# Kernel tuning notes

Hardware: AMD Instinct MI355X
Metric: run time of the kernel (lower is better)

The kernel has to match this reference:

```python
import jax, jax.numpy as jnp
import numpy as np

# ---- model constants (match init_kwargs) ----
N_USERS = 100_000
N_ITEMS = 50_000
N_ENTITIES = 200_000          # items are entities [0, N_ITEMS)
N_REL = 20                    # relations after the +1 shift; rel_weight has N_REL-1 rows
EMB = 64
HOPS = 2
MARGIN_CCL = 0.8
NUM_NEG = 64
ANGLE_W = 0.1
ANGLE_DROP = 0.5              # eval-mode Dropout(ones)*rate == constant rate scaling
N_EDGES = 1_000_000
NNZ = 1_000_000
N_TRIPLETS = 200_000
BATCH = 4096
EPS = 1e-6


def _l2norm(x):
    # torch F.normalize(dim=-1, eps=1e-12)
    return x / jnp.maximum(jnp.linalg.norm(x, axis=-1, keepdims=True), 1e-12)


def setup_inputs() -> dict:
    key = jax.random.key(0)
    ks = jax.random.split(key, 13)
    # xavier_uniform bounds: sqrt(6/(fan_in+fan_out))
    b_all = float(np.sqrt(6.0 / (N_USERS + N_ENTITIES + EMB)))
    b_cf = float(np.sqrt(6.0 / (N_ITEMS + EMB)))
    b_rel = float(np.sqrt(6.0 / (N_REL - 1 + EMB)))
    all_embed = jax.random.uniform(ks[0], (N_USERS + N_ENTITIES, EMB), jnp.float32, -b_all, b_all)
    item_emb_cf = jax.random.uniform(ks[1], (N_ITEMS, EMB), jnp.float32, -b_cf, b_cf)
    rel_weight = jax.random.uniform(ks[2], (N_REL - 1, EMB), jnp.float32, -b_rel, b_rel)
    # D^{-1/2} A row-normalized positive values
    interact_vals = jax.random.uniform(ks[3], (NNZ,), jnp.float32, 0.01, 0.3)
    user = jax.random.randint(ks[4], (BATCH,), 0, N_USERS)
    pos_item = jax.random.randint(ks[5], (BATCH,), 0, N_ITEMS)
    neg_item = jax.random.randint(ks[6], (BATCH, NUM_NEG), 0, N_ITEMS)
    edge_index = jax.random.randint(ks[7], (2, N_EDGES), 0, N_ENTITIES)
    edge_type = jax.random.randint(ks[8], (N_EDGES,), 1, N_REL)  # relations already +1 shifted
    interact_rows = jax.random.randint(ks[9], (NNZ,), 0, N_USERS)
    interact_cols = jax.random.randint(ks[10], (NNZ,), 0, N_ITEMS)  # URM cols live in item range
    triplet_h = jax.random.randint(ks[11], (N_TRIPLETS,), 0, N_ENTITIES)
    triplet_t = jax.random.randint(ks[12], (N_TRIPLETS,), 0, N_ITEMS)
    return dict(all_embed=all_embed, item_emb_cf=item_emb_cf, rel_weight=rel_weight,
                interact_vals=interact_vals, user=user, pos_item=pos_item, neg_item=neg_item,
                edge_index=edge_index, edge_type=edge_type, interact_rows=interact_rows,
                interact_cols=interact_cols, triplet_h=triplet_h, triplet_t=triplet_t)


def _gcn(user_emb, entity_emb, item_cf, rel_weight, edge_index, edge_type, rows, cols, vals):
    """Multi-hop HAKG GraphConv: relation-gated KG scatter-mean + sparse user/CF aggregation."""
    head, tail = edge_index[0], edge_index[1]
    ent_res, usr_res, cf_res = entity_emb, user_emb, item_cf
    cnt = jax.ops.segment_sum(jnp.ones(head.shape, entity_emb.dtype), head, N_ENTITIES)
    denom = jnp.maximum(cnt, 1.0)[:, None]            # scatter_mean denominator
    rel_e = rel_weight[edge_type - 1]                 # [E, D]
    for _ in range(HOPS):
        # KG aggregate: entity_agg[h] = mean_{(h,r,t)} entity[t] * rel[r]
        neigh = entity_emb[tail] * rel_e              # [E, D]
        entity_agg = jax.ops.segment_sum(neigh, head, N_ENTITIES) / denom
        # user aggregate: sparse interact_mat @ entity_emb
        user_agg = jax.ops.segment_sum(vals[:, None] * entity_emb[cols], rows, N_USERS)
        # CF branch (LightGCN-style): R @ item_cf then R^T @ (...)
        u_cf = jax.ops.segment_sum(vals[:, None] * item_cf[cols], rows, N_USERS)
        item_agg_cf = jax.ops.segment_sum(vals[:, None] * u_cf[rows], cols, N_ITEMS)
        entity_emb = _l2norm(entity_agg)
        user_emb = _l2norm(user_agg)
        item_cf = _l2norm(item_agg_cf)
        ent_res = ent_res + entity_emb
        usr_res = usr_res + user_emb
        cf_res = cf_res + item_cf
    return ent_res, usr_res, cf_res


def _half_aperture(u):
    K = 0.1
    sqnu = jnp.clip(jnp.sum(u * u, -1), 0.0, 1.0 - EPS)
    return jnp.arcsin(jnp.clip(K * (1.0 - sqnu) / jnp.sqrt(sqnu), -1.0 + EPS, 1.0 - EPS))


def _angle_at_u(u, v):
    nu = jnp.linalg.norm(u, axis=-1)
    nv = jnp.linalg.norm(v, axis=-1)
    dp = jnp.sum(u * v, -1)
    ed = jnp.linalg.norm(u - v, axis=-1)
    num = dp * (1.0 + nu ** 2) - nu ** 2 * (1.0 + nv ** 2)
    den = nu * ed * jnp.sqrt(jnp.clip(1.0 + nv ** 2 * nu ** 2 - 2.0 * dp, EPS, None)) + EPS
    return jnp.arccos(jnp.clip(num / den, -1.0 + EPS, 1.0 - EPS))


def _contrastive_loss(u_e, pos_e, neg_e, pos_cf, neg_cf):
    B = u_e.shape[0]
    u, p, n = _l2norm(u_e), _l2norm(pos_e), _l2norm(neg_e)
    pcf, ncf = _l2norm(pos_cf), _l2norm(neg_cf)
    ui_pos = jax.nn.relu(2.0 - (jnp.sum(u * p, -1) + jnp.sum(u * pcf, -1)))
    ub = jnp.repeat(u, NUM_NEG, axis=0)               # [B*K, D]
    def neg_loss(nn_):
        s = jax.nn.relu(jnp.sum(ub * nn_, -1) - MARGIN_CCL).reshape(B, NUM_NEG)
        return jnp.sum(s, -1) / (jnp.sum(s > 0, -1).astype(s.dtype) + 1e-5)
    return jnp.mean(ui_pos + neg_loss(n) + neg_loss(ncf))


def reference(all_embed, item_emb_cf, rel_weight, interact_vals, user, pos_item, neg_item,
              edge_index, edge_type, interact_rows, interact_cols, triplet_h, triplet_t):
    user_emb = all_embed[:N_USERS]
    entity_emb = all_embed[N_USERS:]
    ent_g, usr_g, cf_g = _gcn(user_emb, entity_emb, item_emb_cf, rel_weight,
                              edge_index, edge_type, interact_rows, interact_cols, interact_vals)
    flat_neg = neg_item.reshape(-1)
    u_e = usr_g[user]
    loss1 = _contrastive_loss(u_e, ent_g[pos_item], ent_g[flat_neg], cf_g[pos_item], cf_g[flat_neg])
    # angle (hierarchy) loss, vectorized over all cross-type triplets
    hs = entity_emb[triplet_h] * ANGLE_DROP
    ts = entity_emb[triplet_t] * ANGLE_DROP
    angle_half = jax.nn.relu(_angle_at_u(hs, ts) - _half_aperture(hs))
    loss2 = ANGLE_W * jnp.sum(angle_half) / N_TRIPLETS
    return loss1 + loss2
```

## Files before the change

### kernel.cpp

```cpp
#include <hip/hip_runtime.h>
#include <math.h>

#define N_USERS    100000
#define N_ITEMS    50000
#define N_ENTITIES 200000
#define N_REL      20
#define EMB        64
#define HOPS       2
#define MARGIN_CCL 0.8f
#define NUM_NEG    64
#define ANGLE_W    0.1f
#define ANGLE_DROP 0.5f
#define N_EDGES    1000000
#define NNZ        1000000
#define N_TRIPLETS 200000
#define BATCH      4096
#define EPSF       1e-6f

#define TILE1 4096
#define NBUCK 196
#define ACAP  8192
#define HBLK  ((N_EDGES + TILE1 - 1) / TILE1)
#define P1B   (3 * HBLK)
#define KGB   (N_ENTITIES / 32)
#define UCFB  (N_USERS / 32)
#define ITEMB ((N_ITEMS + 31) / 32)
#define UBB   (BATCH / 32)
#define ANGB  (N_TRIPLETS / 32)
#define LOSSB (BATCH / 4)
#define CONVE (N_ENTITIES * 16 / 256)
#define CONVI (N_ITEMS * 16 / 256)

typedef _Float16 half4_t __attribute__((ext_vector_type(4)));
typedef _Float16 half8_t __attribute__((ext_vector_type(8)));
typedef float float8_t __attribute__((ext_vector_type(8)));

__device__ inline float4 h2f(half4_t h) {
    return make_float4((float)h.x, (float)h.y, (float)h.z, (float)h.w);
}
__device__ inline half4_t f2h(float4 f) {
    half4_t h; h.x = (_Float16)f.x; h.y = (_Float16)f.y;
    h.z = (_Float16)f.z; h.w = (_Float16)f.w; return h;
}
__device__ inline float8_t h8_to_f8(half8_t h) { return __builtin_convertvector(h, float8_t); }
__device__ inline half8_t f8_to_h8(float8_t f) { return __builtin_convertvector(f, half8_t); }
__device__ inline half8_t h8_zero() {
    half8_t z;
    #pragma unroll
    for (int i = 0; i < 8; ++i) z[i] = (_Float16)0.0f;
    return z;
}
__device__ inline float sum_sq8(float8_t f) {
    float s = 0.f;
    #pragma unroll
    for (int i = 0; i < 8; ++i) s += f[i] * f[i];
    return s;
}
__device__ inline float dot8(float8_t a, float8_t b) {
    float s = 0.f;
    #pragma unroll
    for (int i = 0; i < 8; ++i) s += a[i] * b[i];
    return s;
}
__device__ inline float8_t f8_from2(float4 lo, float4 hi) {
    float8_t f;
    f[0] = lo.x; f[1] = lo.y; f[2] = lo.z; f[3] = lo.w;
    f[4] = hi.x; f[5] = hi.y; f[6] = hi.z; f[7] = hi.w;
    return f;
}
__device__ inline float grp_red8(float v) {
    v += __shfl_xor(v, 1, 64); v += __shfl_xor(v, 2, 64); v += __shfl_xor(v, 4, 64);
    return v;
}
__device__ inline float dot4(float4 a, float4 b) {
    return a.x * b.x + a.y * b.y + a.z * b.z + a.w * b.w;
}
__device__ inline float grp_red16(float v) {
    v += __shfl_xor(v, 1, 64); v += __shfl_xor(v, 2, 64);
    v += __shfl_xor(v, 4, 64); v += __shfl_xor(v, 8, 64);
    return v;
}
__device__ inline float cross_grp_scalar(float v) {
    v += __shfl_xor(v, 16, 64); v += __shfl_xor(v, 32, 64);
    return v;
}
__device__ inline int f32_to_h16bits(float v) {
    _Float16 h = (_Float16)v;
    return (int)__builtin_bit_cast(unsigned short, h);
}
__device__ inline _Float16 h16_from_bits(int b) {
    return __builtin_bit_cast(_Float16, (unsigned short)(b & 0xFFFF));
}

__global__ void __launch_bounds__(256) prep_kernel(
        int* __restrict__ bcur_e, int* __restrict__ bcur_u, int* __restrict__ bcur_i) {
    int t = threadIdx.x;
    if (t < NBUCK) {
        bcur_e[t] = t * ACAP;
        bcur_u[t] = t * ACAP;
        bcur_i[t] = t * ACAP;
    }
}

__device__ inline void angle_body(int ablk, int t, const half8_t* __restrict__ ent_h,
                                  const int* __restrict__ th, const int* __restrict__ tt,
                                  float* sb, float* __restrict__ l2blk) {
    int o = t & 7;
    int grp = t >> 3;
    int trip = ablk * 32 + grp;
    int h = th[trip], t2 = tt[trip];
    float8_t hv = h8_to_f8(ent_h[h * 8 + o]);
    float8_t tv = h8_to_f8(ent_h[t2 * 8 + o]);
    hv *= ANGLE_DROP;
    tv *= ANGLE_DROP;
    float8_t dv = hv - tv;
    float s_hh = grp_red8(sum_sq8(hv));
    float s_tt = grp_red8(sum_sq8(tv));
    float s_ht = grp_red8(dot8(hv, tv));
    float s_dd = grp_red8(sum_sq8(dv));
    if (o == 0) {
        float nu = sqrtf(s_hh);
        float ed = sqrtf(s_dd);
        float sqnu = fminf(fmaxf(s_hh, 0.0f), 1.0f - EPSF);
        float ha_arg = fminf(fmaxf(0.1f * (1.0f - sqnu) / sqrtf(sqnu), -1.0f + EPSF), 1.0f - EPSF);
        float half_ap = asinf(ha_arg);
        float num = s_ht * (1.0f + s_hh) - s_hh * (1.0f + s_tt);
        float den = nu * ed * sqrtf(fmaxf(1.0f + s_tt * s_hh - 2.0f * s_ht, EPSF)) + EPSF;
        float ang = acosf(fminf(fmaxf(num / den, -1.0f + EPSF), 1.0f - EPSF));
        sb[grp] = fmaxf(ang - half_ap, 0.0f);
    }
    __syncthreads();
    if (t == 0) {
        float tot = 0.f;
        #pragma unroll
        for (int i = 0; i < 32; ++i) tot += sb[i];
        l2blk[ablk] = tot;
    }
}

__global__ void __launch_bounds__(256) phase1_sort(
        const int* __restrict__ head, const int* __restrict__ tail,
        const int* __restrict__ etype, const int* __restrict__ rows,
        const int* __restrict__ cols, const float* __restrict__ vals,
        int* __restrict__ bcur_e, int* __restrict__ bcur_u, int* __restrict__ bcur_i,
        int* __restrict__ keys_ping, int* __restrict__ kg_ping,
        int2* __restrict__ u_ping, int2* __restrict__ i_ping,
        const float4* __restrict__ ent0, const float4* __restrict__ cf0,
        half4_t* __restrict__ ent_a4, half4_t* __restrict__ cf16a4) {
    __shared__ int2 pay_st[TILE1];
    __shared__ int lhist[256], lstart[256], lcur[256], gbase[256];
    __shared__ int wsum[4], wpre[4];
    int bx = blockIdx.x, t = threadIdx.x;
    if (bx >= P1B) {
        int cb = bx - P1B;
        if (cb < CONVE) { int i = cb * 256 + t; ent_a4[i] = f2h(ent0[i]); }
        else            { int i = (cb - CONVE) * 256 + t; cf16a4[i] = f2h(cf0[i]); }
        return;
    }
    int seg = bx / HBLK;
    int tb  = bx % HBLK;
    int tstart = tb * TILE1;
    int valid = min(TILE1, N_EDGES - tstart);
    const int* karr = (seg == 0) ? head : (seg == 1) ? rows : cols;
    int shift = (seg == 0) ? 10 : (seg == 1) ? 9 : 8;
    int* bcur = (seg == 0) ? bcur_e : (seg == 1) ? bcur_u : bcur_i;
    lhist[t] = 0;
    __syncthreads();
    for (int i = t; i < valid; i += 256) atomicAdd(&lhist[karr[tstart + i] >> shift], 1);
    __syncthreads();
    int v = lhist[t];
    int lane = t & 63, wv = t >> 6;
    int sc = v;
    #pragma unroll
    for (int d = 1; d < 64; d <<= 1) {
        int x = __shfl_up(sc, d, 64);
        if (lane >= d) sc += x;
    }
    if (lane == 63) wsum[wv] = sc;
    __syncthreads();
    if (t == 0) {
        int a = 0;
        #pragma unroll
        for (int i = 0; i < 4; ++i) { wpre[i] = a; a += wsum[i]; }
    }
    __syncthreads();
    int excl = sc + wpre[wv] - v;
    lstart[t] = excl;
    lcur[t] = excl;
    gbase[t] = atomicAdd(&bcur[t], v);
    __syncthreads();
    if (seg == 0) {
        int* key_st = (int*)pay_st;
        int* ps = key_st + TILE1;
        for (int i = t; i < valid; i += 256) {
            int h = head[tstart + i];
            int p = tail[tstart + i] | ((etype[tstart + i] - 1) << 18);
            int sp = atomicAdd(&lcur[h >> 10], 1);
            key_st[sp] = h;
            ps[sp] = p;
        }
        __syncthreads();
        for (int j = t; j < valid; j += 256) {
            int k = key_st[j];
            int b = k >> 10;
            int pos = gbase[b] + (j - lstart[b]);
            keys_ping[pos] = k;
            kg_ping[pos] = ps[j];
        }
    } else {
        int2* pay = (seg == 1) ? u_ping : i_ping;
        for (int i = t; i < valid; i += 256) {
            int k = karr[tstart + i];
            int bkt = k >> shift;
            int px;
            if (seg == 1) px = cols[tstart + i] | ((k & 511) << 16);
            else          px = rows[tstart + i] | ((k & 255) << 17);
            int py = f32_to_h16bits(vals[tstart + i]) | (bkt << 16);
            int sp = atomicAdd(&lcur[bkt], 1);
            pay_st[sp] = make_int2(px, py);
        }
        __syncthreads();
        for (int j = t; j < valid; j += 256) {
            int2 p = pay_st[j];
            int bb = (p.y >> 16) & 0xFF;
            int pos = gbase[bb] + (j - lstart[bb]);
            pay[pos] = p;
        }
    }
}

__global__ void __launch_bounds__(256) phase2_all(
        const int* __restrict__ bcur_e, const int* __restrict__ keys_ping,
        const int* __restrict__ kg_ping, int* __restrict__ kg_pack, int* __restrict__ off_e,
        const int* __restrict__ bcur_u, const int2* __restrict__ u_ping,
        int2* __restrict__ u_pack, int* __restrict__ off_u,
        const int* __restrict__ bcur_i, const int2* __restrict__ i_ping,
        int2* __restrict__ i_pack, int* __restrict__ off_i) {
    __shared__ int hist[1024];
    __shared__ int wsum[4], wpre[4];
    int seg = blockIdx.x / NBUCK;
    int b   = blockIdx.x % NBUCK;
    int t = threadIdx.x;
    int bins  = (seg == 0) ? 1024 : (seg == 1) ? 512 : 256;
    int shift = (seg == 0) ? 10 : (seg == 1) ? 9 : 8;
    int n_rows = (seg == 0) ? N_ENTITIES : (seg == 1) ? N_USERS : N_ITEMS;
    const int* bcur = (seg == 0) ? bcur_e : (seg == 1) ? bcur_u : bcur_i;
    int* off = (seg == 0) ? off_e : (seg == 1) ? off_u : off_i;
    int rs = b << shift;
    int re = min(rs + bins, n_rows);
    int nr = re - rs;
    int base = b * ACAP;
    int len = bcur[b] - base;
    for (int r = t; r < bins; r += 256) hist[r] = 0;
    __syncthreads();
    if (seg == 0) {
        for (int j = t; j < len; j += 256) atomicAdd(&hist[keys_ping[base + j] - rs], 1);
    } else if (seg == 1) {
        for (int j = t; j < len; j += 256) atomicAdd(&hist[(u_ping[base + j].x >> 16) & 511], 1);
    } else {
        for (int j = t; j < len; j += 256) atomicAdd(&hist[(i_ping[base + j].x >> 17) & 255], 1);
    }
    __syncthreads();
    int own = bins >> 8;
    int c[4]; int tot = 0;
    #pragma unroll
    for (int i = 0; i < 4; ++i) { c[i] = (i < own) ? hist[t * own + i] : 0; tot += c[i]; }
    int lane = t & 63, wv = t >> 6;
    int sc = tot;
    #pragma unroll
    for (int d = 1; d < 64; d <<= 1) {
        int x = __shfl_up(sc, d, 64);
        if (lane >= d) sc += x;
    }
    if (lane == 63) wsum[wv] = sc;
    __syncthreads();
    if (t == 0) {
        int a = 0;
        #pragma unroll
        for (int i = 0; i < 4; ++i) { wpre[i] = a; a += wsum[i]; }
    }
    __syncthreads();
    int run = sc + wpre[wv] - tot;
    #pragma unroll
    for (int i = 0; i < 4; ++i) { if (i < own) { hist[t * own + i] = run; run += c[i]; } }
    __syncthreads();
    for (int r = t; r < nr; r += 256) off[rs + b + r] = base + hist[r];
    if (t == 0) off[rs + b + nr] = base + len;
    __syncthreads();
    if (seg == 0) {
        for (int j = t; j < len; j += 256) {
            int k = keys_ping[base + j];
            int slot = atomicAdd(&hist[k - rs], 1);
            kg_pack[base + slot] = kg_ping[base + j];
        }
    } else if (seg == 1) {
        for (int j = t; j < len; j += 256) {
            int2 p = u_ping[base + j];
            int slot = atomicAdd(&hist[(p.x >> 16) & 511], 1);
            u_pack[base + slot] = p;
        }
    } else {
        for (int j = t; j < len; j += 256) {
            int2 p = i_ping[base + j];
            int slot = atomicAdd(&hist[(p.x >> 17) & 255], 1);
            i_pack[base + slot] = p;
        }
    }
}

__device__ inline void kg0_body(int bid, int t, const int* __restrict__ off,
                                const int* __restrict__ pack, half8_t* srel,
                                const float* __restrict__ relw,
                                const half8_t* __restrict__ src, half8_t* __restrict__ dst,
                                half8_t* __restrict__ res, const float4* __restrict__ res_init) {
    if (t < (N_REL - 1) * 8) {
        int rel = t >> 3, o = t & 7;
        const float4* r4 = (const float4*)relw;
        srel[rel * 9 + o] = f8_to_h8(f8_from2(r4[rel * 16 + o * 2], r4[rel * 16 + o * 2 + 1]));
    }
    __syncthreads();
    int row = bid * 32 + (t >> 3);
    int o = t & 7;
    int idx = row + (row >> 10);
    int s = off[idx], e = off[idx + 1];
    half8_t acc = h8_zero();
    int k = s;
    for (; k + 2 <= e; k += 2) {
        int p0 = pack[k], p1 = pack[k + 1];
        half8_t a0 = src[(p0 & 0x3FFFF) * 8 + o];
        half8_t b0 = srel[(p0 >> 18) * 9 + o];
        half8_t a1 = src[(p1 & 0x3FFFF) * 8 + o];
        half8_t b1 = srel[(p1 >> 18) * 9 + o];
        acc += a0 * b0;
        acc += a1 * b1;
    }
    if (k < e) {
        int p0 = pack[k];
        acc += src[(p0 & 0x3FFFF) * 8 + o] * srel[(p0 >> 18) * 9 + o];
    }
    float8_t f = h8_to_f8(acc);
    f *= 1.0f / fmaxf((float)(e - s), 1.0f);
    float ss = grp_red8(sum_sq8(f));
    f *= 1.0f / fmaxf(sqrtf(ss), 1e-12f);
    dst[row * 8 + o] = f8_to_h8(f);
    if (row < N_ITEMS) {
        float8_t rr = f8_from2(res_init[row * 16 + o * 2], res_init[row * 16 + o * 2 + 1]);
        rr += f;
        res[row * 8 + o] = f8_to_h8(rr);
    }
}

__device__ inline void kg2_body(int bid, int t, const int* __restrict__ off,
                                const int* __restrict__ pack, half8_t* srel,
                                const float* __restrict__ relw,
                                const half8_t* __restrict__ src, half8_t* __restrict__ res) {
    if (t < (N_REL - 1) * 8) {
        int rel = t >> 3, o = t & 7;
        const float4* r4 = (const float4*)relw;
        srel[rel * 9 + o] = f8_to_h8(f8_from2(r4[rel * 16 + o * 2], r4[rel * 16 + o * 2 + 1]));
    }
    __syncthreads();
    int row = bid * 32 + (t >> 3);
    if (row >= N_ITEMS) return;
    int o = t & 7;
    int idx = row + (row >> 10);
    int s = off[idx], e = off[idx + 1];
    half8_t acc = h8_zero();
    int k = s;
    for (; k + 2 <= e; k += 2) {
        int p0 = pack[k], p1 = pack[k + 1];
        half8_t a0 = src[(p0 & 0x3FFFF) * 8 + o];
        half8_t b0 = srel[(p0 >> 18) * 9 + o];
        half8_t a1 = src[(p1 & 0x3FFFF) * 8 + o];
        half8_t b1 = srel[(p1 >> 18) * 9 + o];
        acc += a0 * b0;
        acc += a1 * b1;
    }
    if (k < e) {
        int p0 = pack[k];
        acc += src[(p0 & 0x3FFFF) * 8 + o] * srel[(p0 >> 18) * 9 + o];
    }
    float8_t f = h8_to_f8(acc);
    f *= 1.0f / fmaxf((float)(e - s), 1.0f);
    float ss = grp_red8(sum_sq8(f));
    f *= 1.0f / fmaxf(sqrtf(ss), 1e-12f);
    float8_t rr = h8_to_f8(res[row * 8 + o]);
    rr += f;
    float s2 = grp_red8(sum_sq8(rr));
    rr *= 1.0f / fmaxf(sqrtf(s2), 1e-12f);
    res[row * 8 + o] = f8_to_h8(rr);
}

__device__ inline void ucf_body(int bid, int t, const int* __restrict__ off,
                                const int2* __restrict__ u_pack,
                                const half8_t* __restrict__ cf16,
                                half8_t* __restrict__ ucf) {
    int row = bid * 32 + (t >> 3);
    int o = t & 7;
    int idx = row + (row >> 9);
    int s = off[idx], e = off[idx + 1];
    half8_t acc = h8_zero();
    int k = s;
    for (; k + 2 <= e; k += 2) {
        int2 p0 = u_pack[k], p1 = u_pack[k + 1];
        _Float16 v0 = h16_from_bits(p0.y);
        _Float16 v1 = h16_from_bits(p1.y);
        acc += cf16[(p0.x & 0xFFFF) * 8 + o] * v0;
        acc += cf16[(p1.x & 0xFFFF) * 8 + o] * v1;
    }
    if (k < e) {
        int2 p0 = u_pack[k];
        acc += cf16[(p0.x & 0xFFFF) * 8 + o] * h16_from_bits(p0.y);
    }
    ucf[row * 8 + o] = acc;
}

__device__ inline void ubatch_body(int bid, int t, const int* __restrict__ user,
                                   const int* __restrict__ off,
                                   const int2* __restrict__ u_pack,
                                   const half8_t* __restrict__ ent_a,
                                   const half8_t* __restrict__ ent_b,
                                   const float4* __restrict__ usr0f,
                                   half8_t* __restrict__ usr_b) {
    int g = t >> 3, o = t & 7;
    int b = bid * 32 + g;
    int uid = user[b];
    int idx = uid + (uid >> 9);
    int s = off[idx], e = off[idx + 1];
    half8_t acc1 = h8_zero(), acc2 = h8_zero();
    int k = s;
    for (; k + 2 <= e; k += 2) {
        int2 p0 = u_pack[k], p1 = u_pack[k + 1];
        int c0 = (p0.x & 0xFFFF) * 8 + o;
        int c1 = (p1.x & 0xFFFF) * 8 + o;
        _Float16 v0 = h16_from_bits(p0.y);
        _Float16 v1 = h16_from_bits(p1.y);
        acc1 += ent_a[c0] * v0;
        acc2 += ent_b[c0] * v0;
        acc1 += ent_a[c1] * v1;
        acc2 += ent_b[c1] * v1;
    }
    if (k < e) {
        int2 p0 = u_pack[k];
        int c0 = (p0.x & 0xFFFF) * 8 + o;
        _Float16 v0 = h16_from_bits(p0.y);
        acc1 += ent_a[c0] * v0;
        acc2 += ent_b[c0] * v0;
    }
    float8_t f1 = h8_to_f8(acc1);
    float ss1 = grp_red8(sum_sq8(f1));
    f1 *= 1.0f / fmaxf(sqrtf(ss1), 1e-12f);
    float8_t u0 = f8_from2(usr0f[uid * 16 + o * 2], usr0f[uid * 16 + o * 2 + 1]);
    float8_t r1 = h8_to_f8(f8_to_h8(u0 + f1));
    float8_t f2 = h8_to_f8(acc2);
    float ss2 = grp_red8(sum_sq8(f2));
    f2 *= 1.0f / fmaxf(sqrtf(ss2), 1e-12f);
    float8_t r = r1 + f2;
    float s3 = grp_red8(sum_sq8(r));
    r *= 1.0f / fmaxf(sqrtf(s3), 1e-12f);
    usr_b[b * 8 + o] = f8_to_h8(r);
}

__device__ inline void item_body(int bid, int t, const int* __restrict__ off,
                                 const int2* __restrict__ i_pack,
                                 const half8_t* __restrict__ ucf,
                                 half8_t* __restrict__ cf_nxt, half8_t* __restrict__ res,
                                 const float4* __restrict__ res_init, int first, int last) {
    int row = bid * 32 + (t >> 3);
    int o = t & 7;
    if (row >= N_ITEMS) return;
    int idx = row + (row >> 8);
    int s = off[idx], e = off[idx + 1];
    half8_t acc = h8_zero();
    int k = s;
    for (; k + 2 <= e; k += 2) {
        int2 p0 = i_pack[k], p1 = i_pack[k + 1];
        _Float16 v0 = h16_from_bits(p0.y);
        _Float16 v1 = h16_from_bits(p1.y);
        acc += ucf[(p0.x & 0x1FFFF) * 8 + o] * v0;
        acc += ucf[(p1.x & 0x1FFFF) * 8 + o] * v1;
    }
    if (k < e) {
        int2 p0 = i_pack[k];
        acc += ucf[(p0.x & 0x1FFFF) * 8 + o] * h16_from_bits(p0.y);
    }
    float8_t f = h8_to_f8(acc);
    float ss = grp_red8(sum_sq8(f));
    f *= 1.0f / fmaxf(sqrtf(ss), 1e-12f);
    if (!last) cf_nxt[row * 8 + o] = f8_to_h8(f);
    float8_t rr;
    if (first) rr = f8_from2(res_init[row * 16 + o * 2], res_init[row * 16 + o * 2 + 1]);
    else       rr = h8_to_f8(res[row * 8 + o]);
    rr += f;
    if (last) {
        float s2 = grp_red8(sum_sq8(rr));
        rr *= 1.0f / fmaxf(sqrtf(s2), 1e-12f);
    }
    res[row * 8 + o] = f8_to_h8(rr);
}

__device__ inline void loss_ent_body(int b, int t,
                                     const int* __restrict__ pos, const int* __restrict__ neg,
                                     const half4_t* __restrict__ usrb4,
                                     const half4_t* __restrict__ ent4,
                                     float* __restrict__ dpe, float* __restrict__ l1pe) {
    int lane = t & 63;
    int g = lane >> 4, q = lane & 15;
    int pid = pos[b];
    float4 u = h2f(usrb4[b * 16 + q]);
    float4 p = h2f(ent4[pid * 16 + q]);
    float dpe_v = grp_red16(dot4(u, p));
    float sum_n = 0.f, cnt_n = 0.f;
    const int* nb = neg + b * NUM_NEG;
    for (int j = 0; j < NUM_NEG; j += 8) {
        int n0 = nb[j + g], n1 = nb[j + 4 + g];
        float dn0 = grp_red16(dot4(u, h2f(ent4[n0 * 16 + q])));
        float dn1 = grp_red16(dot4(u, h2f(ent4[n1 * 16 + q])));
        float s0 = fmaxf(dn0 - MARGIN_CCL, 0.f); sum_n += s0; if (s0 > 0.f) cnt_n += 1.f;
        float s1 = fmaxf(dn1 - MARGIN_CCL, 0.f); sum_n += s1; if (s1 > 0.f) cnt_n += 1.f;
    }
    sum_n = cross_grp_scalar(sum_n); cnt_n = cross_grp_scalar(cnt_n);
    if (lane == 0) {
        dpe[b] = dpe_v;
        l1pe[b] = sum_n / (cnt_n + 1e-5f);
    }
}

__global__ void __launch_bounds__(256) loss_cf_kernel(
        const int* __restrict__ pos, const int* __restrict__ neg,
        const half4_t* __restrict__ usrb4, const half4_t* __restrict__ cf4,
        const float* __restrict__ dpe, const float* __restrict__ l1pe,
        float* __restrict__ l1p) {
    int b = blockIdx.x * 4 + (threadIdx.x >> 6);
    int lane = threadIdx.x & 63;
    int g = lane >> 4, q = lane & 15;
    int pid = pos[b];
    float4 u = h2f(usrb4[b * 16 + q]);
    float4 pc = h2f(cf4[pid * 16 + q]);
    float dpc = grp_red16(dot4(u, pc));
    float sum_c = 0.f, cnt_c = 0.f;
    const int* nb = neg + b * NUM_NEG;
    for (int j = 0; j < NUM_NEG; j += 8) {
        int n0 = nb[j + g], n1 = nb[j + 4 + g];
        float dc0 = grp_red16(dot4(u, h2f(cf4[n0 * 16 + q])));
        float dc1 = grp_red16(dot4(u, h2f(cf4[n1 * 16 + q])));
        float t0 = fmaxf(dc0 - MARGIN_CCL, 0.f); sum_c += t0; if (t0 > 0.f) cnt_c += 1.f;
        float t1 = fmaxf(dc1 - MARGIN_CCL, 0.f); sum_c += t1; if (t1 > 0.f) cnt_c += 1.f;
    }
    sum_c = cross_grp_scalar(sum_c); cnt_c = cross_grp_scalar(cnt_c);
    if (lane == 0) {
        float ui_pos = fmaxf(2.0f - dpe[b] - dpc, 0.0f);
        l1p[b] = ui_pos + l1pe[b] + sum_c / (cnt_c + 1e-5f);
    }
}

__global__ void __launch_bounds__(256) fused_h0(
        const int* __restrict__ off_e, const int* __restrict__ kg_pack,
        const float* __restrict__ relw, const half8_t* __restrict__ ent_a,
        half8_t* __restrict__ ent_b, half8_t* __restrict__ ent_res,
        const float4* __restrict__ ent0f,
        const int* __restrict__ off_u, const int2* __restrict__ u_pack,
        const half8_t* __restrict__ cf16_a, half8_t* __restrict__ ucf,
        const int* __restrict__ th, const int* __restrict__ tt,
        float* __restrict__ l2blk) {
    __shared__ half8_t srel[(N_REL - 1) * 9];
    __shared__ float sb[32];
    int bx = blockIdx.x, t = threadIdx.x;
    if (bx < KGB) {
        kg0_body(bx, t, off_e, kg_pack, srel, relw, ent_a, ent_b, ent_res, ent0f);
    } else if (bx < KGB + UCFB) {
        ucf_body(bx - KGB, t, off_u, u_pack, cf16_a, ucf);
    } else {
        angle_body(bx - KGB - UCFB, t, ent_a, th, tt, sb, l2blk);
    }
}

__global__ void __launch_bounds__(256) fused_ik(
        const int* __restrict__ off_e, const int* __restrict__ kg_pack,
        const float* __restrict__ relw, const half8_t* __restrict__ ent_b,
        half8_t* __restrict__ ent_res,
        const int* __restrict__ off_i, const int2* __restrict__ i_pack,
        const half8_t* __restrict__ ucf, half8_t* __restrict__ cf16_b,
        half8_t* __restrict__ cf_res, const float4* __restrict__ cf0f,
        const int* __restrict__ user, const int* __restrict__ off_u,
        const int2* __restrict__ u_pack, const half8_t* __restrict__ ent_a,
        const float4* __restrict__ usr0f, half8_t* __restrict__ usr_b) {
    __shared__ half8_t srel[(N_REL - 1) * 9];
    int bx = blockIdx.x, t = threadIdx.x;
    if (bx < ITEMB) {
        kg2_body(bx, t, off_e, kg_pack, srel, relw, ent_b, ent_res);
    } else if (bx < 2 * ITEMB) {
        item_body(bx - ITEMB, t, off_i, i_pack, ucf, cf16_b, cf_res, cf0f, 1, 0);
    } else {
        ubatch_body(bx - 2 * ITEMB, t, user, off_u, u_pack, ent_a, ent_b, usr0f, usr_b);
    }
}

__global__ void __launch_bounds__(256) fused_u1_loss(
        const int* __restrict__ off_u, const int2* __restrict__ u_pack,
        const half8_t* __restrict__ cf16_b, half8_t* __restrict__ ucf,
        const int* __restrict__ pos, const int* __restrict__ neg,
        const half4_t* __restrict__ usrb4, const half4_t* __restrict__ ent4,
        float* __restrict__ dpe, float* __restrict__ l1pe) {
    int bx = blockIdx.x, t = threadIdx.x;
    if (bx < UCFB) {
        ucf_body(bx, t, off_u, u_pack, cf16_b, ucf);
    } else {
        int b = (bx - UCFB) * 4 + (t >> 6);
        loss_ent_body(b, t, pos, neg, usrb4, ent4, dpe, l1pe);
    }
}

__global__ void __launch_bounds__(256) item_h1(
        const int* __restrict__ off_i, const int2* __restrict__ i_pack,
        const half8_t* __restrict__ ucf, half8_t* __restrict__ cf_res,
        const float4* __restrict__ cf0f) {
    item_body(blockIdx.x, threadIdx.x, off_i, i_pack, ucf, (half8_t*)0, cf_res, cf0f, 0, 1);
}

__global__ void finalize_kernel(const float* __restrict__ l1p, const float* __restrict__ l2b,
                                float* __restrict__ out) {
    __shared__ float sb[1024];
    float a1 = 0.f;
    for (int i = threadIdx.x; i < BATCH; i += 1024) a1 += l1p[i];
    float a2 = 0.f;
    for (int i = threadIdx.x; i < ANGB; i += 1024) a2 += l2b[i];
    sb[threadIdx.x] = a1 / (float)BATCH + ANGLE_W * a2 / (float)N_TRIPLETS;
    __syncthreads();
    for (int s = 512; s > 0; s >>= 1) {
        if (threadIdx.x < s) sb[threadIdx.x] += sb[threadIdx.x + s];
        __syncthreads();
    }
    if (threadIdx.x == 0) out[0] = sb[0];
}

extern "C" void kernel_launch(void* const* d_in, const int* in_sizes, int n_in,
                              void* d_out, int out_size, void* d_ws, size_t ws_size,
                              hipStream_t stream) {
    const float* all_embed = (const float*)d_in[0];
    const float* item_cf0  = (const float*)d_in[1];
    const float* relw      = (const float*)d_in[2];
    const float* vals      = (const float*)d_in[3];
    const int* user        = (const int*)d_in[4];
    const int* pos_item    = (const int*)d_in[5];
    const int* neg_item    = (const int*)d_in[6];
    const int* edge_head   = (const int*)d_in[7];
    const int* edge_tail   = edge_head + N_EDGES;
    const int* etype       = (const int*)d_in[8];
    const int* irows       = (const int*)d_in[9];
    const int* icols       = (const int*)d_in[10];
    const int* th          = (const int*)d_in[11];
    const int* tt          = (const int*)d_in[12];
    float* out             = (float*)d_out;

    char* base = (char*)d_ws;
    size_t woff = 0;
    auto alloc = [&](size_t bytes) -> void* {
        void* p = base + woff;
        woff = (woff + bytes + 255) & ~(size_t)255;
        return p;
    };
    const size_t ping_ui = (size_t)NBUCK * ACAP * 8;
    const size_t ping_kg = (size_t)NBUCK * ACAP * 4;

    half8_t* ent_a   = (half8_t*)alloc((size_t)N_ENTITIES * EMB * 2);
    half8_t* ent_b   = (half8_t*)alloc(2 * ping_ui);
    half8_t* cf16_a  = (half8_t*)alloc((size_t)N_ITEMS * EMB * 2);
    half8_t* cf16_b  = (half8_t*)alloc(ping_kg);
    half8_t* ucf     = (half8_t*)alloc((size_t)N_USERS * EMB * 2);
    half8_t* ent_res = (half8_t*)alloc((size_t)N_ITEMS * EMB * 2);
    half8_t* cf_res  = (half8_t*)alloc((size_t)N_ITEMS * EMB * 2);
    half8_t* usr_b   = (half8_t*)alloc((size_t)BATCH * EMB * 2);
    int2* u_pack     = (int2*)alloc(ping_ui);
    int2* i_pack     = (int2*)alloc(ping_ui);
    int* kg_pack     = (int*)alloc(ping_kg);
    float* l1p       = (float*)alloc((size_t)BATCH * 4);
    float* dpe       = (float*)alloc((size_t)BATCH * 4);
    float* l1pe      = (float*)alloc((size_t)BATCH * 4);
    float* l2blk     = (float*)alloc((size_t)ANGB * 4);
    int* off_e       = (int*)alloc((size_t)(N_ENTITIES + NBUCK + 1) * 4);
    int* off_u       = (int*)alloc((size_t)(N_USERS + NBUCK + 1) * 4);
    int* off_i       = (int*)alloc((size_t)(N_ITEMS + NBUCK + 1) * 4);
    int* bcur_e      = (int*)alloc(256 * 4);
    int* bcur_u      = (int*)alloc(256 * 4);
    int* bcur_i      = (int*)alloc(256 * 4);

    int2* u_ping   = (int2*)ent_b;
    int2* i_ping   = (int2*)((char*)ent_b + ping_ui);
    int* kg_ping   = (int*)cf16_b;
    int* keys_ping = (int*)ucf;

    const float* ent0 = all_embed + (size_t)N_USERS * EMB;

    prep_kernel<<<1, 256, 0, stream>>>(bcur_e, bcur_u, bcur_i);
    phase1_sort<<<P1B + CONVE + CONVI, 256, 0, stream>>>(
        edge_head, edge_tail, etype, irows, icols, vals,
        bcur_e, bcur_u, bcur_i, keys_ping, kg_ping, u_ping, i_ping,
        (const float4*)ent0, (const float4*)item_cf0, (half4_t*)ent_a, (half4_t*)cf16_a);
    phase2_all<<<3 * NBUCK, 256, 0, stream>>>(bcur_e, keys_ping, kg_ping, kg_pack, off_e,
                                              bcur_u, u_ping, u_pack, off_u,
                                              bcur_i, i_ping, i_pack, off_i);
    fused_h0<<<KGB + UCFB + ANGB, 256, 0, stream>>>(
        off_e, kg_pack, relw, ent_a, ent_b, ent_res, (const float4*)ent0,
        off_u, u_pack, cf16_a, ucf, th, tt, l2blk);
    fused_ik<<<2 * ITEMB + UBB, 256, 0, stream>>>(
        off_e, kg_pack, relw, ent_b, ent_res,
        off_i, i_pack, ucf, cf16_b, cf_res, (const float4*)item_cf0,
        user, off_u, u_pack, ent_a, (const float4*)all_embed, usr_b);
    fused_u1_loss<<<UCFB + LOSSB, 256, 0, stream>>>(
        off_u, u_pack, cf16_b, ucf, pos_item, neg_item,
        (const half4_t*)usr_b, (const half4_t*)ent_res, dpe, l1pe);
    item_h1<<<ITEMB, 256, 0, stream>>>(off_i, i_pack, ucf, cf_res,
                                       (const float4*)item_cf0);
    loss_cf_kernel<<<LOSSB, 256, 0, stream>>>(pos_item, neg_item,
                                              (const half4_t*)usr_b, (const half4_t*)cf_res,
                                              dpe, l1pe, l1p);
    finalize_kernel<<<1, 1024, 0, stream>>>(l1p, l2blk, out);
}
```

Measured before the change: 357.9 us.

## Move angle loss into phase2, replace prep kernel with memset, unroll gathers by four

```diff
diff --git a/kernel.cpp b/kernel.cpp
--- a/kernel.cpp
+++ b/kernel.cpp
@@ -90,16 +90,6 @@
 }
 __device__ inline _Float16 h16_from_bits(int b) {
     return __builtin_bit_cast(_Float16, (unsigned short)(b & 0xFFFF));
-}
-
-__global__ void __launch_bounds__(256) prep_kernel(
-        int* __restrict__ bcur_e, int* __restrict__ bcur_u, int* __restrict__ bcur_i) {
-    int t = threadIdx.x;
-    if (t < NBUCK) {
-        bcur_e[t] = t * ACAP;
-        bcur_u[t] = t * ACAP;
-        bcur_i[t] = t * ACAP;
-    }
 }
 
 __device__ inline void angle_body(int ablk, int t, const half8_t* __restrict__ ent_h,
@@ -187,7 +177,7 @@
     int excl = sc + wpre[wv] - v;
     lstart[t] = excl;
     lcur[t] = excl;
-    gbase[t] = atomicAdd(&bcur[t], v);
+    gbase[t] = t * ACAP + atomicAdd(&bcur[t], v);
     __syncthreads();
     if (seg == 0) {
         int* key_st = (int*)pay_st;
@@ -229,18 +219,25 @@
     }
 }
 
-__global__ void __launch_bounds__(256) phase2_all(
+__global__ void __launch_bounds__(256) phase2_angle(
         const int* __restrict__ bcur_e, const int* __restrict__ keys_ping,
         const int* __restrict__ kg_ping, int* __restrict__ kg_pack, int* __restrict__ off_e,
         const int* __restrict__ bcur_u, const int2* __restrict__ u_ping,
         int2* __restrict__ u_pack, int* __restrict__ off_u,
         const int* __restrict__ bcur_i, const int2* __restrict__ i_ping,
-        int2* __restrict__ i_pack, int* __restrict__ off_i) {
+        int2* __restrict__ i_pack, int* __restrict__ off_i,
+        const half8_t* __restrict__ ent_a, const int* __restrict__ th,
+        const int* __restrict__ tt, float* __restrict__ l2blk) {
     __shared__ int hist[1024];
     __shared__ int wsum[4], wpre[4];
+    __shared__ float sb[32];
+    int t = threadIdx.x;
+    if (blockIdx.x >= 3 * NBUCK) {
+        angle_body(blockIdx.x - 3 * NBUCK, t, ent_a, th, tt, sb, l2blk);
+        return;
+    }
     int seg = blockIdx.x / NBUCK;
     int b   = blockIdx.x % NBUCK;
-    int t = threadIdx.x;
     int bins  = (seg == 0) ? 1024 : (seg == 1) ? 512 : 256;
     int shift = (seg == 0) ? 10 : (seg == 1) ? 9 : 8;
     int n_rows = (seg == 0) ? N_ENTITIES : (seg == 1) ? N_USERS : N_ITEMS;
@@ -250,7 +247,7 @@
     int re = min(rs + bins, n_rows);
     int nr = re - rs;
     int base = b * ACAP;
-    int len = bcur[b] - base;
+    int len = bcur[b];
     for (int r = t; r < bins; r += 256) hist[r] = 0;
     __syncthreads();
     if (seg == 0) {
@@ -325,16 +322,18 @@
     int s = off[idx], e = off[idx + 1];
     half8_t acc = h8_zero();
     int k = s;
-    for (; k + 2 <= e; k += 2) {
-        int p0 = pack[k], p1 = pack[k + 1];
+    for (; k + 4 <= e; k += 4) {
+        int p0 = pack[k], p1 = pack[k + 1], p2 = pack[k + 2], p3 = pack[k + 3];
         half8_t a0 = src[(p0 & 0x3FFFF) * 8 + o];
-        half8_t b0 = srel[(p0 >> 18) * 9 + o];
         half8_t a1 = src[(p1 & 0x3FFFF) * 8 + o];
-        half8_t b1 = srel[(p1 >> 18) * 9 + o];
-        acc += a0 * b0;
-        acc += a1 * b1;
-    }
-    if (k < e) {
+        half8_t a2 = src[(p2 & 0x3FFFF) * 8 + o];
+        half8_t a3 = src[(p3 & 0x3FFFF) * 8 + o];
+        acc += a0 * srel[(p0 >> 18) * 9 + o];
+        acc += a1 * srel[(p1 >> 18) * 9 + o];
+        acc += a2 * srel[(p2 >> 18) * 9 + o];
+        acc += a3 * srel[(p3 >> 18) * 9 + o];
+    }
+    for (; k < e; ++k) {
         int p0 = pack[k];
         acc += src[(p0 & 0x3FFFF) * 8 + o] * srel[(p0 >> 18) * 9 + o];
     }
@@ -367,16 +366,18 @@
     int s = off[idx], e = off[idx + 1];
     half8_t acc = h8_zero();
     int k = s;
-    for (; k + 2 <= e; k += 2) {
-        int p0 = pack[k], p1 = pack[k + 1];
+    for (; k + 4 <= e; k += 4) {
+        int p0 = pack[k], p1 = pack[k + 1], p2 = pack[k + 2], p3 = pack[k + 3];
         half8_t a0 = src[(p0 & 0x3FFFF) * 8 + o];
-        half8_t b0 = srel[(p0 >> 18) * 9 + o];
         half8_t a1 = src[(p1 & 0x3FFFF) * 8 + o];
-        half8_t b1 = srel[(p1 >> 18) * 9 + o];
-        acc += a0 * b0;
-        acc += a1 * b1;
-    }
-    if (k < e) {
+        half8_t a2 = src[(p2 & 0x3FFFF) * 8 + o];
+        half8_t a3 = src[(p3 & 0x3FFFF) * 8 + o];
+        acc += a0 * srel[(p0 >> 18) * 9 + o];
+        acc += a1 * srel[(p1 >> 18) * 9 + o];
+        acc += a2 * srel[(p2 >> 18) * 9 + o];
+        acc += a3 * srel[(p3 >> 18) * 9 + o];
+    }
+    for (; k < e; ++k) {
         int p0 = pack[k];
         acc += src[(p0 & 0x3FFFF) * 8 + o] * srel[(p0 >> 18) * 9 + o];
     }
@@ -401,14 +402,18 @@
     int s = off[idx], e = off[idx + 1];
     half8_t acc = h8_zero();
     int k = s;
-    for (; k + 2 <= e; k += 2) {
-        int2 p0 = u_pack[k], p1 = u_pack[k + 1];
-        _Float16 v0 = h16_from_bits(p0.y);
-        _Float16 v1 = h16_from_bits(p1.y);
-        acc += cf16[(p0.x & 0xFFFF) * 8 + o] * v0;
-        acc += cf16[(p1.x & 0xFFFF) * 8 + o] * v1;
-    }
-    if (k < e) {
+    for (; k + 4 <= e; k += 4) {
+        int2 p0 = u_pack[k], p1 = u_pack[k + 1], p2 = u_pack[k + 2], p3 = u_pack[k + 3];
+        half8_t c0 = cf16[(p0.x & 0xFFFF) * 8 + o];
+        half8_t c1 = cf16[(p1.x & 0xFFFF) * 8 + o];
+        half8_t c2 = cf16[(p2.x & 0xFFFF) * 8 + o];
+        half8_t c3 = cf16[(p3.x & 0xFFFF) * 8 + o];
+        acc += c0 * h16_from_bits(p0.y);
+        acc += c1 * h16_from_bits(p1.y);
+        acc += c2 * h16_from_bits(p2.y);
+        acc += c3 * h16_from_bits(p3.y);
+    }
+    for (; k < e; ++k) {
         int2 p0 = u_pack[k];
         acc += cf16[(p0.x & 0xFFFF) * 8 + o] * h16_from_bits(p0.y);
     }
@@ -429,18 +434,26 @@
     int s = off[idx], e = off[idx + 1];
     half8_t acc1 = h8_zero(), acc2 = h8_zero();
     int k = s;
-    for (; k + 2 <= e; k += 2) {
-        int2 p0 = u_pack[k], p1 = u_pack[k + 1];
+    for (; k + 4 <= e; k += 4) {
+        int2 p0 = u_pack[k], p1 = u_pack[k + 1], p2 = u_pack[k + 2], p3 = u_pack[k + 3];
         int c0 = (p0.x & 0xFFFF) * 8 + o;
         int c1 = (p1.x & 0xFFFF) * 8 + o;
+        int c2 = (p2.x & 0xFFFF) * 8 + o;
+        int c3 = (p3.x & 0xFFFF) * 8 + o;
+        half8_t ea0 = ent_a[c0], eb0 = ent_b[c0];
+        half8_t ea1 = ent_a[c1], eb1 = ent_b[c1];
+        half8_t ea2 = ent_a[c2], eb2 = ent_b[c2];
+        half8_t ea3 = ent_a[c3], eb3 = ent_b[c3];
         _Float16 v0 = h16_from_bits(p0.y);
         _Float16 v1 = h16_from_bits(p1.y);
-        acc1 += ent_a[c0] * v0;
-        acc2 += ent_b[c0] * v0;
-        acc1 += ent_a[c1] * v1;
-        acc2 += ent_b[c1] * v1;
-    }
-    if (k < e) {
+        _Float16 v2 = h16_from_bits(p2.y);
+        _Float16 v3 = h16_from_bits(p3.y);
+        acc1 += ea0 * v0; acc2 += eb0 * v0;
+        acc1 += ea1 * v1; acc2 += eb1 * v1;
+        acc1 += ea2 * v2; acc2 += eb2 * v2;
+        acc1 += ea3 * v3; acc2 += eb3 * v3;
+    }
+    for (; k < e; ++k) {
         int2 p0 = u_pack[k];
         int c0 = (p0.x & 0xFFFF) * 8 + o;
         _Float16 v0 = h16_from_bits(p0.y);
@@ -473,14 +486,18 @@
     int s = off[idx], e = off[idx + 1];
     half8_t acc = h8_zero();
     int k = s;
-    for (; k + 2 <= e; k += 2) {
-        int2 p0 = i_pack[k], p1 = i_pack[k + 1];
-        _Float16 v0 = h16_from_bits(p0.y);
-        _Float16 v1 = h16_from_bits(p1.y);
-        acc += ucf[(p0.x & 0x1FFFF) * 8 + o] * v0;
-        acc += ucf[(p1.x & 0x1FFFF) * 8 + o] * v1;
-    }
-    if (k < e) {
+    for (; k + 4 <= e; k += 4) {
+        int2 p0 = i_pack[k], p1 = i_pack[k + 1], p2 = i_pack[k + 2], p3 = i_pack[k + 3];
+        half8_t c0 = ucf[(p0.x & 0x1FFFF) * 8 + o];
+        half8_t c1 = ucf[(p1.x & 0x1FFFF) * 8 + o];
+        half8_t c2 = ucf[(p2.x & 0x1FFFF) * 8 + o];
+        half8_t c3 = ucf[(p3.x & 0x1FFFF) * 8 + o];
+        acc += c0 * h16_from_bits(p0.y);
+        acc += c1 * h16_from_bits(p1.y);
+        acc += c2 * h16_from_bits(p2.y);
+        acc += c3 * h16_from_bits(p3.y);
+    }
+    for (; k < e; ++k) {
         int2 p0 = i_pack[k];
         acc += ucf[(p0.x & 0x1FFFF) * 8 + o] * h16_from_bits(p0.y);
     }
@@ -512,12 +529,20 @@
     float dpe_v = grp_red16(dot4(u, p));
     float sum_n = 0.f, cnt_n = 0.f;
     const int* nb = neg + b * NUM_NEG;
-    for (int j = 0; j < NUM_NEG; j += 8) {
-        int n0 = nb[j + g], n1 = nb[j + 4 + g];
-        float dn0 = grp_red16(dot4(u, h2f(ent4[n0 * 16 + q])));
-        float dn1 = grp_red16(dot4(u, h2f(ent4[n1 * 16 + q])));
+    for (int j = 0; j < NUM_NEG; j += 16) {
+        int n0 = nb[j + g], n1 = nb[j + 4 + g], n2 = nb[j + 8 + g], n3 = nb[j + 12 + g];
+        float4 e0 = h2f(ent4[n0 * 16 + q]);
+        float4 e1 = h2f(ent4[n1 * 16 + q]);
+        float4 e2 = h2f(ent4[n2 * 16 + q]);
+        float4 e3 = h2f(ent4[n3 * 16 + q]);
+        float dn0 = grp_red16(dot4(u, e0));
+        float dn1 = grp_red16(dot4(u, e1));
+        float dn2 = grp_red16(dot4(u, e2));
+        float dn3 = grp_red16(dot4(u, e3));
         float s0 = fmaxf(dn0 - MARGIN_CCL, 0.f); sum_n += s0; if (s0 > 0.f) cnt_n += 1.f;
         float s1 = fmaxf(dn1 - MARGIN_CCL, 0.f); sum_n += s1; if (s1 > 0.f) cnt_n += 1.f;
+        float s2 = fmaxf(dn2 - MARGIN_CCL, 0.f); sum_n += s2; if (s2 > 0.f) cnt_n += 1.f;
+        float s3 = fmaxf(dn3 - MARGIN_CCL, 0.f); sum_n += s3; if (s3 > 0.f) cnt_n += 1.f;
     }
     sum_n = cross_grp_scalar(sum_n); cnt_n = cross_grp_scalar(cnt_n);
     if (lane == 0) {
@@ -540,12 +565,20 @@
     float dpc = grp_red16(dot4(u, pc));
     float sum_c = 0.f, cnt_c = 0.f;
     const int* nb = neg + b * NUM_NEG;
-    for (int j = 0; j < NUM_NEG; j += 8) {
-        int n0 = nb[j + g], n1 = nb[j + 4 + g];
-        float dc0 = grp_red16(dot4(u, h2f(cf4[n0 * 16 + q])));
-        float dc1 = grp_red16(dot4(u, h2f(cf4[n1 * 16 + q])));
+    for (int j = 0; j < NUM_NEG; j += 16) {
+        int n0 = nb[j + g], n1 = nb[j + 4 + g], n2 = nb[j + 8 + g], n3 = nb[j + 12 + g];
+        float4 e0 = h2f(cf4[n0 * 16 + q]);
+        float4 e1 = h2f(cf4[n1 * 16 + q]);
+        float4 e2 = h2f(cf4[n2 * 16 + q]);
+        float4 e3 = h2f(cf4[n3 * 16 + q]);
+        float dc0 = grp_red16(dot4(u, e0));
+        float dc1 = grp_red16(dot4(u, e1));
+        float dc2 = grp_red16(dot4(u, e2));
+        float dc3 = grp_red16(dot4(u, e3));
         float t0 = fmaxf(dc0 - MARGIN_CCL, 0.f); sum_c += t0; if (t0 > 0.f) cnt_c += 1.f;
         float t1 = fmaxf(dc1 - MARGIN_CCL, 0.f); sum_c += t1; if (t1 > 0.f) cnt_c += 1.f;
+        float t2 = fmaxf(dc2 - MARGIN_CCL, 0.f); sum_c += t2; if (t2 > 0.f) cnt_c += 1.f;
+        float t3 = fmaxf(dc3 - MARGIN_CCL, 0.f); sum_c += t3; if (t3 > 0.f) cnt_c += 1.f;
     }
     sum_c = cross_grp_scalar(sum_c); cnt_c = cross_grp_scalar(cnt_c);
     if (lane == 0) {
@@ -560,18 +593,13 @@
         half8_t* __restrict__ ent_b, half8_t* __restrict__ ent_res,
         const float4* __restrict__ ent0f,
         const int* __restrict__ off_u, const int2* __restrict__ u_pack,
-        const half8_t* __restrict__ cf16_a, half8_t* __restrict__ ucf,
-        const int* __restrict__ th, const int* __restrict__ tt,
-        float* __restrict__ l2blk) {
+        const half8_t* __restrict__ cf16_a, half8_t* __restrict__ ucf) {
     __shared__ half8_t srel[(N_REL - 1) * 9];
-    __shared__ float sb[32];
     int bx = blockIdx.x, t = threadIdx.x;
     if (bx < KGB) {
         kg0_body(bx, t, off_e, kg_pack, srel, relw, ent_a, ent_b, ent_res, ent0f);
-    } else if (bx < KGB + UCFB) {
+    } else {
         ucf_body(bx - KGB, t, off_u, u_pack, cf16_a, ucf);
-    } else {
-        angle_body(bx - KGB - UCFB, t, ent_a, th, tt, sb, l2blk);
     }
 }
 
@@ -681,9 +709,10 @@
     int* off_e       = (int*)alloc((size_t)(N_ENTITIES + NBUCK + 1) * 4);
     int* off_u       = (int*)alloc((size_t)(N_USERS + NBUCK + 1) * 4);
     int* off_i       = (int*)alloc((size_t)(N_ITEMS + NBUCK + 1) * 4);
-    int* bcur_e      = (int*)alloc(256 * 4);
-    int* bcur_u      = (int*)alloc(256 * 4);
-    int* bcur_i      = (int*)alloc(256 * 4);
+    int* bcur_all    = (int*)alloc(3 * 256 * 4);
+    int* bcur_e      = bcur_all;
+    int* bcur_u      = bcur_all + 256;
+    int* bcur_i      = bcur_all + 512;
 
     int2* u_ping   = (int2*)ent_b;
     int2* i_ping   = (int2*)((char*)ent_b + ping_ui);
@@ -692,17 +721,19 @@
 
     const float* ent0 = all_embed + (size_t)N_USERS * EMB;
 
-    prep_kernel<<<1, 256, 0, stream>>>(bcur_e, bcur_u, bcur_i);
+    hipMemsetAsync(bcur_all, 0, 3 * 256 * 4, stream);
     phase1_sort<<<P1B + CONVE + CONVI, 256, 0, stream>>>(
         edge_head, edge_tail, etype, irows, icols, vals,
         bcur_e, bcur_u, bcur_i, keys_ping, kg_ping, u_ping, i_ping,
         (const float4*)ent0, (const float4*)item_cf0, (half4_t*)ent_a, (half4_t*)cf16_a);
-    phase2_all<<<3 * NBUCK, 256, 0, stream>>>(bcur_e, keys_ping, kg_ping, kg_pack, off_e,
-                                              bcur_u, u_ping, u_pack, off_u,
-                                              bcur_i, i_ping, i_pack, off_i);
-    fused_h0<<<KGB + UCFB + ANGB, 256, 0, stream>>>(
+    phase2_angle<<<3 * NBUCK + ANGB, 256, 0, stream>>>(
+        bcur_e, keys_ping, kg_ping, kg_pack, off_e,
+        bcur_u, u_ping, u_pack, off_u,
+        bcur_i, i_ping, i_pack, off_i,
+        (const half8_t*)ent_a, th, tt, l2blk);
+    fused_h0<<<KGB + UCFB, 256, 0, stream>>>(
         off_e, kg_pack, relw, ent_a, ent_b, ent_res, (const float4*)ent0,
-        off_u, u_pack, cf16_a, ucf, th, tt, l2blk);
+        off_u, u_pack, cf16_a, ucf);
     fused_ik<<<2 * ITEMB + UBB, 256, 0, stream>>>(
         off_e, kg_pack, relw, ent_b, ent_res,
         off_i, i_pack, ucf, cf16_b, cf_res, (const float4*)item_cf0,
```

Result: no change. 351.1 us (-1.9%).
